# Performance work log

Hardware: AMD Instinct MI355X
Metric: run time of the kernel (lower is better)

Reference implementation:

```python
import jax, jax.numpy as jnp
import numpy as np

N, E, C, Z = 20000, 320000, 64, 10
NLM, NB, P = 9, 8, 4          # (lmax=2 -> 9 lm comps), 8 Bessel, 4 contraction paths
RMAX, AVG = 5.0, 16.0         # radial cutoff, avg_num_neighbors
L_OF_LM = jnp.array([0, 1, 1, 1, 2, 2, 2, 2, 2])  # which l each lm component belongs to


def _sph_harm(u):
    """Component-normalized real spherical harmonics, lmax=2. u: [E,3] unit vectors."""
    x, y, z = u[:, 0], u[:, 1], u[:, 2]
    s3, s5, s15 = jnp.sqrt(3.0), jnp.sqrt(5.0), jnp.sqrt(15.0)
    return jnp.stack([
        jnp.ones_like(x),
        s3 * x, s3 * y, s3 * z,
        s15 * x * y, s15 * y * z, 0.5 * s5 * (3.0 * z * z - 1.0),
        s15 * x * z, 0.5 * s15 * (x * x - y * y),
    ], axis=-1)  # [E, 9]


def _forward(positions, atomic_indices, edge_index, W_embed, W_up,
             mlp_w1, mlp_w2, mlp_w3, mlp_w4, U3, U2, U1, Wc3, Wc2, Wc1, W_out):
    sender, receiver = edge_index[0], edge_index[1]
    # edge vectors / lengths (shifts == 0)
    vec = positions[receiver] - positions[sender]               # [E,3]
    r = jnp.sqrt(jnp.sum(vec * vec, axis=-1) + 1e-12)           # [E]
    Y = _sph_harm(vec / r[:, None])                             # [E,9]
    # Bessel radial basis * polynomial cutoff (p=6)
    n = jnp.arange(1, NB + 1, dtype=positions.dtype)
    bessel = jnp.sqrt(2.0 / RMAX) * jnp.sin(n[None, :] * jnp.pi * r[:, None] / RMAX) / r[:, None]
    u = jnp.clip(r / RMAX, 0.0, 1.0)
    p = 6.0
    fcut = 1.0 - 0.5 * (p + 1) * (p + 2) * u**6 + p * (p + 2) * u**7 - 0.5 * p * (p + 1) * u**8
    edge_feats = bessel * fcut[:, None]                         # [E,8]
    # per-edge tensor-product weights: SiLU MLP, no biases (MACE FullyConnectedNet)
    f = jax.nn.silu(edge_feats @ mlp_w1)
    f = jax.nn.silu(f @ mlp_w2)
    f = jax.nn.silu(f @ mlp_w3)
    tpw = (f @ mlp_w4).reshape(-1, 3, C)                        # [E, n_l=3, C]
    # node embedding (one-hot linear) + linear_up, e3nn 1/sqrt(fan_in) norm
    h = W_embed[atomic_indices] / jnp.sqrt(jnp.asarray(Z, positions.dtype))  # [N,C]
    h = (h @ W_up) / jnp.sqrt(jnp.asarray(C, positions.dtype))               # [N,C]
    # channelwise tensor product 64x0e (x) (0e+1o+2e): gather-TP
    w_lm = tpw[:, L_OF_LM, :]                                   # [E,9,C]
    mji = h[sender][:, :, None] * jnp.swapaxes(w_lm, 1, 2) * Y[:, None, :]  # [E,C,9]
    # scatter-sum messages to receivers
    message = jax.ops.segment_sum(mji, receiver, num_segments=N) / AVG       # [N,C,9]
    x = message  # reshape() output: [N, C, lm]
    # symmetric product contraction (correlation=3), element-dependent weights
    W3n, W2n, W1n = Wc3[atomic_indices], Wc2[atomic_indices], Wc1[atomic_indices]  # [N,P,C]
    out = jnp.einsum('ijkp,npc,nci->ncjk', U3, W3n, x)          # [N,C,9,9]
    c2 = jnp.einsum('jkp,npc->ncjk', U2, W2n) + out
    out = jnp.einsum('ncjk,nck->ncj', c2, x)                    # [N,C,9]
    c1 = jnp.einsum('jp,npc->ncj', U1, W1n) + out
    out = jnp.einsum('ncj,ncj->nc', c1, x)                      # [N,C] invariant output
    return (out @ W_out) / jnp.sqrt(jnp.asarray(C, positions.dtype))


def setup_inputs() -> dict:
    key = jax.random.key(0)
    ks = jax.random.split(key, 16)
    return {
        'positions': jax.random.normal(ks[0], (N, 3), jnp.float32),
        'atomic_indices': jax.random.randint(ks[1], (N,), 0, Z),
        'edge_index': jax.random.randint(ks[2], (2, E), 0, N),
        'W_embed': jax.random.normal(ks[3], (Z, C), jnp.float32),
        'W_up': jax.random.normal(ks[4], (C, C), jnp.float32),
        'mlp_w1': jax.random.normal(ks[5], (NB, 64), jnp.float32) / np.sqrt(NB),
        'mlp_w2': jax.random.normal(ks[6], (64, 64), jnp.float32) / 8.0,
        'mlp_w3': jax.random.normal(ks[7], (64, 64), jnp.float32) / 8.0,
        'mlp_w4': jax.random.normal(ks[8], (64, 3 * C), jnp.float32) / 8.0,
        'U3': jax.random.normal(ks[9], (NLM, NLM, NLM, P), jnp.float32) * 0.1,
        'U2': jax.random.normal(ks[10], (NLM, NLM, P), jnp.float32) * 0.1,
        'U1': jax.random.normal(ks[11], (NLM, P), jnp.float32) * 0.1,
        'Wc3': jax.random.normal(ks[12], (Z, P, C), jnp.float32) * 0.1,
        'Wc2': jax.random.normal(ks[13], (Z, P, C), jnp.float32) * 0.1,
        'Wc1': jax.random.normal(ks[14], (Z, P, C), jnp.float32) * 0.1,
        'W_out': jax.random.normal(ks[15], (C, C), jnp.float32),
    }


def reference(positions, atomic_indices, edge_index, W_embed, W_up,
              mlp_w1, mlp_w2, mlp_w3, mlp_w4, U3, U2, U1, Wc3, Wc2, Wc1, W_out):
    return _forward(positions, atomic_indices, edge_index, W_embed, W_up,
                    mlp_w1, mlp_w2, mlp_w3, mlp_w4, U3, U2, U1, Wc3, Wc2, Wc1, W_out)
```

## Files before the change

### kernel.cpp

```cpp
#include <hip/hip_runtime.h>
#include <hip/hip_bf16.h>

typedef unsigned short u16;
typedef unsigned int u32;
typedef __attribute__((ext_vector_type(8))) short bf16x8;
typedef __attribute__((ext_vector_type(4))) float f32x4;

#define NN 20000
#define NE 320000

#define WP_H     256
#define WP_U1    3072
#define WP_U2    3328
#define WP_U3    4096
#define WP_CUR   7168
#define WP_POSF  87168
#define WP_WB    407168
#define WP_EL16  452224

__device__ __forceinline__ float bf2f(u16 u){ return __uint_as_float(((u32)u) << 16); }
__device__ __forceinline__ u16 f2bf(float f){
  u32 u = __float_as_uint(f);
  u32 r = (u + 0x7fffu + ((u >> 16) & 1u)) >> 16;
  return (u16)r;
}
__device__ __forceinline__ u16 f2bfa(float f){
  return (u16)((__float_as_uint(f) + 0x8000u) >> 16);
}
__device__ __forceinline__ u32 pk2bf(float a, float b){
  __hip_bfloat162 h = __float22bfloat162_rn(make_float2(a, b));
  return *(u32*)&h;
}
__device__ __forceinline__ float silu_f(float v){
  return v * __builtin_amdgcn_rcpf(1.0f + __expf(-v));
}
__device__ __forceinline__ float ldf(const void* p, int i, int bf){
  return bf ? bf2f(((const u16*)p)[i]) : ((const float*)p)[i];
}
__device__ __forceinline__ f32x4 mfma16(bf16x8 a, bf16x8 b, f32x4 c){
  return __builtin_amdgcn_mfma_f32_16x16x32_bf16(a, b, c, 0, 0, 0);
}

#define WAVE_SYNC() do { \
  __builtin_amdgcn_wave_barrier(); \
  asm volatile("s_waitcnt lgkmcnt(0)" ::: "memory"); \
  __builtin_amdgcn_wave_barrier(); \
} while (0)

#define SOFT_FENCE() do { \
  __builtin_amdgcn_wave_barrier(); \
  asm volatile("" ::: "memory"); \
  __builtin_amdgcn_wave_barrier(); \
} while (0)

__device__ __forceinline__ int sniff_wave(const u32* wu, int lane){
  u32 w = wu[lane];
  u32 e = (w >> 7) & 0xFFu;
  unsigned long long m = __ballot(e >= 0x60u && e <= 0x86u);
  return (__popcll(m) > 37) ? 1 : 0;
}

extern "C" __global__ __launch_bounds__(256)
void k_prep_pad(const void* __restrict__ We, const void* __restrict__ Wu,
                const void* __restrict__ U3, const void* __restrict__ U2, const void* __restrict__ U1,
                const void* __restrict__ w1, const void* __restrict__ w2,
                const void* __restrict__ w3, const void* __restrict__ w4,
                const void* __restrict__ pos, const int* __restrict__ eidx,
                float* __restrict__ Hws, float* __restrict__ U3ws,
                float* __restrict__ U2ws, float* __restrict__ U1ws,
                u16* __restrict__ wbws, float4* __restrict__ posf,
                int* __restrict__ cur, u16* __restrict__ el16)
{
  int tid = threadIdx.x;
  int b = blockIdx.x;
  int bf = sniff_wave((const u32*)Wu, tid & 63);

  {
    int e = b*256 + tid;
    int r = eidx[NE + e];
    int s = eidx[e];
    int slot = atomicAdd(&cur[r], 1);
    if (slot < 64) el16[(r << 6) + slot] = (u16)s;
  }

  if (b == 0){
    for (int t = tid; t < 36; t += 256) U1ws[t] = ldf(U1, t, bf);
    for (int t = tid; t < 45; t += 256){
      int j = 0, rem = t;
      for (;;){ int cnt = 9 - j; if (rem < cnt) break; rem -= cnt; ++j; }
      int k = j + rem;
      for (int p = 0; p < 4; ++p){
        float v = ldf(U2, (j*9 + k)*4 + p, bf);
        if (k > j) v += ldf(U2, (k*9 + j)*4 + p, bf);
        U2ws[t*4 + p] = v;
      }
    }
    for (int t = tid; t < 165; t += 256){
      int i = 0, rem = t;
      for (;;){ int m = 9 - i; int cnt = m*(m+1)/2; if (rem < cnt) break; rem -= cnt; ++i; }
      int j = i;
      for (;;){ int cnt = 9 - j; if (rem < cnt) break; rem -= cnt; ++j; }
      int k = j + rem;
      int pm[6][3] = {{i,j,k},{i,k,j},{j,i,k},{j,k,i},{k,i,j},{k,j,i}};
      float acc[4] = {0,0,0,0};
      for (int m = 0; m < 6; ++m){
        bool dup = false;
        for (int mm = 0; mm < m; ++mm)
          if (pm[mm][0]==pm[m][0] && pm[mm][1]==pm[m][1] && pm[mm][2]==pm[m][2]) dup = true;
        if (!dup){
          int base = ((pm[m][0]*9 + pm[m][1])*9 + pm[m][2])*4;
          for (int p = 0; p < 4; ++p) acc[p] += ldf(U3, base + p, bf);
        }
      }
      for (int p = 0; p < 4; ++p) U3ws[t*4 + p] = acc[p];
    }
  } else if (b <= 88){
    int idx = (b - 1)*256 + tid;
    int f = idx >> 9;
    int L = (idx >> 3) & 63;
    int j = idx & 7;
    int kl = ((L >> 4) << 3) + j;
    int n16 = L & 15;
    float v;
    if (f < 4){
      v = (kl < 8) ? ldf(w1, kl*64 + (f*16 + n16), bf) : 0.f;
    } else if (f < 12){
      int g = f - 4; int t = g >> 1, q = g & 1;
      v = ldf(w2, (q*32 + kl)*64 + (t*16 + n16), bf);
    } else if (f < 20){
      int g = f - 12; int t = g >> 1, q = g & 1;
      v = ldf(w3, (q*32 + kl)*64 + (t*16 + n16), bf);
    } else {
      int g = f - 20; int lt = g >> 1, q = g & 1;
      int l = lt >> 2, ct = lt & 3;
      v = ldf(w4, (q*32 + kl)*192 + (l*64 + ct*16 + n16), bf);
    }
    wbws[idx] = f2bf(v);
  } else if (b <= 167){
    int i = (b - 89)*256 + tid;
    if (i < NN){
      float4 v;
      v.x = ldf(pos, 3*i+0, bf); v.y = ldf(pos, 3*i+1, bf); v.z = ldf(pos, 3*i+2, bf); v.w = 0.f;
      posf[i] = v;
    }
  } else if (b <= 177){
    int z = b - 168;
    int c = tid;
    if (c < 64){
      float s = 0.f;
      for (int k = 0; k < 64; ++k) s += ldf(We, z*64 + k, bf) * ldf(Wu, k*64 + c, bf);
      Hws[z*64 + c] = s * 0.0395284708f;
    }
  }
}

__device__ __forceinline__ void edge_geom(float4 pr, float4 ps, float* ef, float* Y)
{
  float vx = pr.x - ps.x, vy = pr.y - ps.y, vz = pr.z - ps.z;
  float r2 = vx*vx + vy*vy + vz*vz + 1e-12f;
  float rinv = rsqrtf(r2);
  float r = r2 * rinv;
  float ux = vx*rinv, uy = vy*rinv, uz = vz*rinv;
  const float s3 = 1.7320508076f, s5 = 2.2360679775f, s15 = 3.8729833462f;
  Y[0] = 1.0f;
  Y[1] = s3*ux; Y[2] = s3*uy; Y[3] = s3*uz;
  Y[4] = s15*ux*uy; Y[5] = s15*uy*uz;
  Y[6] = 0.5f*s5*(3.0f*uz*uz - 1.0f);
  Y[7] = s15*ux*uz;
  Y[8] = 0.5f*s15*(ux*ux - uy*uy);
  float u = r * 0.2f; u = fminf(u, 1.0f);
  float u2 = u*u, u4 = u2*u2, u6 = u4*u2, u7 = u6*u, u8 = u7*u;
  float fc = 1.0f - 28.0f*u6 + 48.0f*u7 - 21.0f*u8;
  float c0 = 0.63245553203f * fc * rinv;
  float w = 0.62831853072f * r;
  #pragma unroll
  for (int k = 0; k < 8; ++k) ef[k] = c0 * __sinf(w * (float)(k + 1));
}

extern "C" __global__ __launch_bounds__(256, 3)
void k_main(const int* __restrict__ atom,
            const void* __restrict__ Wu,
            const void* __restrict__ Wc3, const void* __restrict__ Wc2, const void* __restrict__ Wc1,
            const void* __restrict__ Woutg,
            const float* __restrict__ Hws, const float* __restrict__ U3ws,
            const float* __restrict__ U2ws, const float* __restrict__ U1ws,
            const float4* __restrict__ posf,
            const int* __restrict__ deg, const u16* __restrict__ el16,
            const u16* __restrict__ wbws, void* __restrict__ outp)
{
  __shared__ __align__(16) u16   wb[12288];
  __shared__ __align__(16) float Hs[10][64];
  __shared__ __align__(16) u16   efb[4][64][8];
  __shared__ __align__(16) u16   zb64[4][64];
  __shared__ __align__(16) u16   act[4][16][64];
  __shared__ __align__(16) u16   Yc[4][64][9];
  __shared__ __align__(16) u16   pfrag[4][4][32][8];

  int tid = threadIdx.x;
  int wv = tid >> 6;
  int lane = tid & 63;
  int bf = sniff_wave((const u32*)Wu, lane);

  for (int t = tid; t < 6144; t += 256) ((u32*)wb)[t] = ((const u32*)wbws)[5120 + t];
  for (int t = tid; t < 640; t += 256) ((float*)Hs)[t] = Hws[t];
  __syncthreads();

  int c0 = lane & 15;
  int qd = lane >> 4;
  int n = blockIdx.x * 4 + wv;
  int cnt = min(deg[n], 64);
  float4 pr = posf[n];

  bf16x8 w1p[4], w2p[8], w3p[8];
  #pragma unroll
  for (int t = 0; t < 4; ++t) w1p[t] = *(const bf16x8*)&wbws[t*512 + lane*8];
  #pragma unroll
  for (int g = 0; g < 8; ++g) w2p[g] = *(const bf16x8*)&wbws[(4+g)*512 + lane*8];
  #pragma unroll
  for (int g = 0; g < 8; ++g) w3p[g] = *(const bf16x8*)&wbws[(12+g)*512 + lane*8];

  int lmap = (c0 == 0) ? 0 : (c0 < 4) ? 1 : 2;
  u32 msk0 = (lmap == 0) ? 0xFFFFFFFFu : 0u;
  u32 msk1 = (lmap == 1) ? 0xFFFFFFFFu : 0u;
  u32 msk2 = (lmap == 2) ? 0xFFFFFFFFu : 0u;

  const f32x4 zero4 = {0.f, 0.f, 0.f, 0.f};
  f32x4 XD[4];
  #pragma unroll
  for (int t = 0; t < 4; ++t) XD[t] = zero4;

  int prow = ((qd >> 1) << 4) + c0;
  int pcol = (qd & 1) << 2;
  int ntile = (cnt + 15) >> 4;

  {
    bool valid = lane < cnt;
    int sid = valid ? (int)el16[(n << 6) + lane] : n;
    float4 ps = posf[sid];
    int z = valid ? atom[sid] : 0;
    float ef[8], Y[9];
    edge_geom(pr, ps, ef, Y);
    if (!valid){
      #pragma unroll
      for (int k = 0; k < 8; ++k) ef[k] = 0.f;
      #pragma unroll
      for (int m = 0; m < 9; ++m) Y[m] = 0.f;
    }
    uint4 pk;
    pk.x = pk2bf(ef[0], ef[1]);
    pk.y = pk2bf(ef[2], ef[3]);
    pk.z = pk2bf(ef[4], ef[5]);
    pk.w = pk2bf(ef[6], ef[7]);
    *(uint4*)&efb[wv][lane][0] = pk;
    #pragma unroll
    for (int m = 0; m < 9; ++m) Yc[wv][lane][m] = f2bf(Y[m]);
    zb64[wv][lane] = (u16)z;
  }
  SOFT_FENCE();

  #pragma unroll 1
  for (int t = 0; t < ntile; ++t){
    f32x4 dd[4];

    bf16x8 aF = {0,0,0,0,0,0,0,0};
    if (lane < 16) aF = *(const bf16x8*)&efb[wv][t*16 + lane][0];
    #pragma unroll
    for (int t2 = 0; t2 < 4; ++t2) dd[t2] = mfma16(aF, w1p[t2], zero4);
    #pragma unroll
    for (int t2 = 0; t2 < 4; ++t2)
      #pragma unroll
      for (int r = 0; r < 4; ++r)
        act[wv][qd*4 + r][c0 + 16*t2] = f2bfa(silu_f(dd[t2][r]));
    SOFT_FENCE();

    bf16x8 a0 = *(const bf16x8*)&act[wv][c0][qd*8];
    bf16x8 a1 = *(const bf16x8*)&act[wv][c0][32 + qd*8];
    #pragma unroll
    for (int t2 = 0; t2 < 4; ++t2)
      dd[t2] = mfma16(a1, w2p[t2*2+1], mfma16(a0, w2p[t2*2+0], zero4));
    #pragma unroll
    for (int t2 = 0; t2 < 4; ++t2)
      #pragma unroll
      for (int r = 0; r < 4; ++r)
        act[wv][qd*4 + r][c0 + 16*t2] = f2bfa(silu_f(dd[t2][r]));
    SOFT_FENCE();

    a0 = *(const bf16x8*)&act[wv][c0][qd*8];
    a1 = *(const bf16x8*)&act[wv][c0][32 + qd*8];
    #pragma unroll
    for (int t2 = 0; t2 < 4; ++t2)
      dd[t2] = mfma16(a1, w3p[t2*2+1], mfma16(a0, w3p[t2*2+0], zero4));
    #pragma unroll
    for (int t2 = 0; t2 < 4; ++t2)
      #pragma unroll
      for (int r = 0; r < 4; ++r)
        act[wv][qd*4 + r][c0 + 16*t2] = f2bfa(silu_f(dd[t2][r]));
    SOFT_FENCE();

    a0 = *(const bf16x8*)&act[wv][c0][qd*8];
    a1 = *(const bf16x8*)&act[wv][c0][32 + qd*8];

    u32 yd0 = 0, yd1 = 0, yd2 = 0, yd3 = 0;
    if (lane < 32 && c0 < 9){
      const u16* yr = &Yc[wv][t*16 + ((lane >> 4) << 3)][0];
      yd0 = (u32)yr[0*9 + c0] | ((u32)yr[1*9 + c0] << 16);
      yd1 = (u32)yr[2*9 + c0] | ((u32)yr[3*9 + c0] << 16);
      yd2 = (u32)yr[4*9 + c0] | ((u32)yr[5*9 + c0] << 16);
      yd3 = (u32)yr[6*9 + c0] | ((u32)yr[7*9 + c0] << 16);
    }
    bf16x8 B0, B1, B2;
    { uint4 t0 = {yd0 & msk0, yd1 & msk0, yd2 & msk0, yd3 & msk0};
      uint4 t1 = {yd0 & msk1, yd1 & msk1, yd2 & msk1, yd3 & msk1};
      uint4 t2 = {yd0 & msk2, yd1 & msk2, yd2 & msk2, yd3 & msk2};
      B0 = *(bf16x8*)&t0; B1 = *(bf16x8*)&t1; B2 = *(bf16x8*)&t2; }

    float hv[4][4];
    #pragma unroll
    for (int r = 0; r < 4; ++r){
      int z_e = (int)zb64[wv][t*16 + qd*4 + r];
      #pragma unroll
      for (int ct = 0; ct < 4; ++ct) hv[r][ct] = Hs[z_e][ct*16 + c0];
    }
    #pragma unroll
    for (int l = 0; l < 3; ++l){
      #pragma unroll
      for (int ct = 0; ct < 4; ++ct){
        int f = (l*4 + ct)*2;
        bf16x8 b0 = *(const bf16x8*)&wb[f*512 + lane*8];
        bf16x8 b1 = *(const bf16x8*)&wb[(f+1)*512 + lane*8];
        dd[ct] = mfma16(a1, b1, mfma16(a0, b0, zero4));
      }
      #pragma unroll
      for (int ct = 0; ct < 4; ++ct){
        uint2 pk2;
        pk2.x = pk2bf(hv[0][ct] * dd[ct][0], hv[1][ct] * dd[ct][1]);
        pk2.y = pk2bf(hv[2][ct] * dd[ct][2], hv[3][ct] * dd[ct][3]);
        *(uint2*)&pfrag[wv][ct][prow][pcol] = pk2;
      }
      SOFT_FENCE();
      bf16x8 Bl = (l == 0) ? B0 : (l == 1) ? B1 : B2;
      #pragma unroll
      for (int ct = 0; ct < 4; ++ct){
        bf16x8 aP = {0,0,0,0,0,0,0,0};
        if (lane < 32) aP = *(const bf16x8*)&pfrag[wv][ct][lane][0];
        XD[ct] = mfma16(aP, Bl, XD[ct]);
      }
      SOFT_FENCE();
    }
  }

  float* Xf8 = (float*)&act[wv][0][0];
  float* X8f = (float*)&efb[wv][0][0];
  SOFT_FENCE();
  #pragma unroll
  for (int ct = 0; ct < 4; ++ct)
    #pragma unroll
    for (int r = 0; r < 4; ++r){
      int c = ct*16 + qd*4 + r;
      if (c0 < 8)       Xf8[c*8 + c0] = XD[ct][r];
      else if (c0 == 8) X8f[c]        = XD[ct][r];
    }
  SOFT_FENCE();
  float X[9];
  {
    const float4* xr = (const float4*)&Xf8[lane*8];
    float4 xa = xr[0], xb = xr[1];
    X[0]=xa.x; X[1]=xa.y; X[2]=xa.z; X[3]=xa.w;
    X[4]=xb.x; X[5]=xb.y; X[6]=xb.z; X[7]=xb.w;
    X[8]=X8f[lane];
  }
  #pragma unroll
  for (int m = 0; m < 9; ++m) X[m] *= 0.0625f;

  const float4* U1g = (const float4*)U1ws;
  const float4* U2g = (const float4*)U2ws;
  const float4* U3g = (const float4*)U3ws;
  float s1a[4] = {0,0,0,0}, s2a[4] = {0,0,0,0}, s3a[4] = {0,0,0,0};
  #pragma unroll
  for (int j = 0; j < 9; ++j){
    float4 u = U1g[j];
    s1a[0] += u.x*X[j]; s1a[1] += u.y*X[j]; s1a[2] += u.z*X[j]; s1a[3] += u.w*X[j];
  }
  {
    int t2i = 0;
    #pragma unroll
    for (int j = 0; j < 9; ++j)
      #pragma unroll
      for (int k = j; k < 9; ++k){
        float m = X[j]*X[k];
        float4 u = U2g[t2i]; ++t2i;
        s2a[0] += u.x*m; s2a[1] += u.y*m; s2a[2] += u.z*m; s2a[3] += u.w*m;
      }
  }
  {
    int t3i = 0;
    #pragma unroll
    for (int i = 0; i < 9; ++i)
      #pragma unroll
      for (int j = i; j < 9; ++j){
        float mij = X[i]*X[j];
        #pragma unroll
        for (int k = j; k < 9; ++k){
          float m = mij*X[k];
          float4 u = U3g[t3i]; ++t3i;
          s3a[0] += u.x*m; s3a[1] += u.y*m; s3a[2] += u.z*m; s3a[3] += u.w*m;
        }
      }
  }

  int zn = atom[n];
  float outval = 0.f;
  #pragma unroll
  for (int p = 0; p < 4; ++p){
    int b = (zn*4 + p)*64 + lane;
    outval += ldf(Wc1, b, bf)*s1a[p] + ldf(Wc2, b, bf)*s2a[p] + ldf(Wc3, b, bf)*s3a[p];
  }

  float* xchg = (float*)&act[wv][0][0];
  SOFT_FENCE();
  xchg[lane] = outval;
  SOFT_FENCE();
  float acc = 0.f;
  const float4* pb = (const float4*)xchg;
  if (bf){
    const u16* wg = (const u16*)Woutg;
    #pragma unroll
    for (int cb = 0; cb < 16; ++cb){
      float4 p = pb[cb];
      acc += p.x*bf2f(wg[(4*cb+0)*64 + lane]) + p.y*bf2f(wg[(4*cb+1)*64 + lane])
           + p.z*bf2f(wg[(4*cb+2)*64 + lane]) + p.w*bf2f(wg[(4*cb+3)*64 + lane]);
    }
  } else {
    const float* wg = (const float*)Woutg;
    #pragma unroll
    for (int cb = 0; cb < 16; ++cb){
      float4 p = pb[cb];
      acc += p.x*wg[(4*cb+0)*64 + lane] + p.y*wg[(4*cb+1)*64 + lane]
           + p.z*wg[(4*cb+2)*64 + lane] + p.w*wg[(4*cb+3)*64 + lane];
    }
  }
  acc *= 0.125f;
  if (bf) ((u16*)outp)[n*64 + lane] = f2bf(acc);
  else    ((float*)outp)[n*64 + lane] = acc;
}

extern "C" void kernel_launch(void* const* d_in, const int* in_sizes, int n_in,
                              void* d_out, int out_size, void* d_ws, size_t ws_size,
                              hipStream_t stream)
{
  const void* pos  = d_in[0];
  const int* atom  = (const int*)d_in[1];
  const int* eidx  = (const int*)d_in[2];
  const void* We   = d_in[3];
  const void* Wu   = d_in[4];
  const void* w1g  = d_in[5];
  const void* w2g  = d_in[6];
  const void* w3g  = d_in[7];
  const void* w4g  = d_in[8];
  const void* U3   = d_in[9];
  const void* U2   = d_in[10];
  const void* U1   = d_in[11];
  const void* Wc3  = d_in[12];
  const void* Wc2  = d_in[13];
  const void* Wc1  = d_in[14];
  const void* Wout = d_in[15];

  char* ws = (char*)d_ws;
  float*  Hws   = (float*)(ws + WP_H);
  float*  U1ws  = (float*)(ws + WP_U1);
  float*  U2ws  = (float*)(ws + WP_U2);
  float*  U3ws  = (float*)(ws + WP_U3);
  int*    cur   = (int*)(ws + WP_CUR);
  float4* posf  = (float4*)(ws + WP_POSF);
  u16*    wbws  = (u16*)(ws + WP_WB);
  u16*    el16  = (u16*)(ws + WP_EL16);

  (void)hipMemsetAsync(ws + WP_CUR, 0, 80000, stream);
  k_prep_pad<<<1250, 256, 0, stream>>>(We, Wu, U3, U2, U1, w1g, w2g, w3g, w4g, pos, eidx,
                                       Hws, U3ws, U2ws, U1ws, wbws, posf, cur, el16);
  k_main<<<5000, 256, 0, stream>>>(atom, Wu, Wc3, Wc2, Wc1, Wout,
                                   Hws, U3ws, U2ws, U1ws, posf,
                                   cur, el16, wbws, d_out);
}
```

Baseline: 289.2 us.

## Drop LDS weight staging, read W4 and H from global, swizzle act buffer

Removes the 24KB shared-memory copy of the fourth MLP weight matrix and the H table. Those values are now read directly from global memory, through the cache, inside the tile loop, and the block-wide syncthreads is dropped. The act scratch buffer gets an XOR swizzle to cut LDS bank conflicts, and launch bounds rise to 5 blocks per CU to raise occupancy. The trade-off is more global/L1 traffic per tile and tighter register limits, which could cause spills.

```diff
diff --git a/kernel.cpp b/kernel.cpp
--- a/kernel.cpp
+++ b/kernel.cpp
@@ -40,12 +40,6 @@
 __device__ __forceinline__ f32x4 mfma16(bf16x8 a, bf16x8 b, f32x4 c){
   return __builtin_amdgcn_mfma_f32_16x16x32_bf16(a, b, c, 0, 0, 0);
 }
-
-#define WAVE_SYNC() do { \
-  __builtin_amdgcn_wave_barrier(); \
-  asm volatile("s_waitcnt lgkmcnt(0)" ::: "memory"); \
-  __builtin_amdgcn_wave_barrier(); \
-} while (0)
 
 #define SOFT_FENCE() do { \
   __builtin_amdgcn_wave_barrier(); \
@@ -177,7 +171,7 @@
   for (int k = 0; k < 8; ++k) ef[k] = c0 * __sinf(w * (float)(k + 1));
 }
 
-extern "C" __global__ __launch_bounds__(256, 3)
+extern "C" __global__ __launch_bounds__(256, 5)
 void k_main(const int* __restrict__ atom,
             const void* __restrict__ Wu,
             const void* __restrict__ Wc3, const void* __restrict__ Wc2, const void* __restrict__ Wc1,
@@ -188,11 +182,9 @@
             const int* __restrict__ deg, const u16* __restrict__ el16,
             const u16* __restrict__ wbws, void* __restrict__ outp)
 {
-  __shared__ __align__(16) u16   wb[12288];
-  __shared__ __align__(16) float Hs[10][64];
+  __shared__ __align__(16) u16   act[4][1024];
   __shared__ __align__(16) u16   efb[4][64][8];
   __shared__ __align__(16) u16   zb64[4][64];
-  __shared__ __align__(16) u16   act[4][16][64];
   __shared__ __align__(16) u16   Yc[4][64][9];
   __shared__ __align__(16) u16   pfrag[4][4][32][8];
 
@@ -200,10 +192,6 @@
   int wv = tid >> 6;
   int lane = tid & 63;
   int bf = sniff_wave((const u32*)Wu, lane);
-
-  for (int t = tid; t < 6144; t += 256) ((u32*)wb)[t] = ((const u32*)wbws)[5120 + t];
-  for (int t = tid; t < 640; t += 256) ((float*)Hs)[t] = Hws[t];
-  __syncthreads();
 
   int c0 = lane & 15;
   int qd = lane >> 4;
@@ -211,6 +199,10 @@
   int cnt = min(deg[n], 64);
   float4 pr = posf[n];
 
+  u16* A = &act[wv][0];
+  int swr = qd << 4;
+  int srd = (c0 >> 2) << 4;
+
   bf16x8 w1p[4], w2p[8], w3p[8];
   #pragma unroll
   for (int t = 0; t < 4; ++t) w1p[t] = *(const bf16x8*)&wbws[t*512 + lane*8];
@@ -218,6 +210,8 @@
   for (int g = 0; g < 8; ++g) w2p[g] = *(const bf16x8*)&wbws[(4+g)*512 + lane*8];
   #pragma unroll
   for (int g = 0; g < 8; ++g) w3p[g] = *(const bf16x8*)&wbws[(12+g)*512 + lane*8];
+
+  const u16* w4b = wbws + 20*512 + lane*8;
 
   int lmap = (c0 == 0) ? 0 : (c0 < 4) ? 1 : 2;
   u32 msk0 = (lmap == 0) ? 0xFFFFFFFFu : 0u;
@@ -270,11 +264,11 @@
     for (int t2 = 0; t2 < 4; ++t2)
       #pragma unroll
       for (int r = 0; r < 4; ++r)
-        act[wv][qd*4 + r][c0 + 16*t2] = f2bfa(silu_f(dd[t2][r]));
+        A[(((qd*4 + r) << 6) + c0 + (t2 << 4)) ^ swr] = f2bfa(silu_f(dd[t2][r]));
     SOFT_FENCE();
 
-    bf16x8 a0 = *(const bf16x8*)&act[wv][c0][qd*8];
-    bf16x8 a1 = *(const bf16x8*)&act[wv][c0][32 + qd*8];
+    bf16x8 a0 = *(const bf16x8*)&A[((c0 << 6) + (qd << 3)) ^ srd];
+    bf16x8 a1 = *(const bf16x8*)&A[((c0 << 6) + 32 + (qd << 3)) ^ srd];
     #pragma unroll
     for (int t2 = 0; t2 < 4; ++t2)
       dd[t2] = mfma16(a1, w2p[t2*2+1], mfma16(a0, w2p[t2*2+0], zero4));
@@ -282,11 +276,11 @@
     for (int t2 = 0; t2 < 4; ++t2)
       #pragma unroll
       for (int r = 0; r < 4; ++r)
-        act[wv][qd*4 + r][c0 + 16*t2] = f2bfa(silu_f(dd[t2][r]));
+        A[(((qd*4 + r) << 6) + c0 + (t2 << 4)) ^ swr] = f2bfa(silu_f(dd[t2][r]));
     SOFT_FENCE();
 
-    a0 = *(const bf16x8*)&act[wv][c0][qd*8];
-    a1 = *(const bf16x8*)&act[wv][c0][32 + qd*8];
+    a0 = *(const bf16x8*)&A[((c0 << 6) + (qd << 3)) ^ srd];
+    a1 = *(const bf16x8*)&A[((c0 << 6) + 32 + (qd << 3)) ^ srd];
     #pragma unroll
     for (int t2 = 0; t2 < 4; ++t2)
       dd[t2] = mfma16(a1, w3p[t2*2+1], mfma16(a0, w3p[t2*2+0], zero4));
@@ -294,11 +288,11 @@
     for (int t2 = 0; t2 < 4; ++t2)
       #pragma unroll
       for (int r = 0; r < 4; ++r)
-        act[wv][qd*4 + r][c0 + 16*t2] = f2bfa(silu_f(dd[t2][r]));
+        A[(((qd*4 + r) << 6) + c0 + (t2 << 4)) ^ swr] = f2bfa(silu_f(dd[t2][r]));
     SOFT_FENCE();
 
-    a0 = *(const bf16x8*)&act[wv][c0][qd*8];
-    a1 = *(const bf16x8*)&act[wv][c0][32 + qd*8];
+    a0 = *(const bf16x8*)&A[((c0 << 6) + (qd << 3)) ^ srd];
+    a1 = *(const bf16x8*)&A[((c0 << 6) + 32 + (qd << 3)) ^ srd];
 
     u32 yd0 = 0, yd1 = 0, yd2 = 0, yd3 = 0;
     if (lane < 32 && c0 < 9){
@@ -319,15 +313,15 @@
     for (int r = 0; r < 4; ++r){
       int z_e = (int)zb64[wv][t*16 + qd*4 + r];
       #pragma unroll
-      for (int ct = 0; ct < 4; ++ct) hv[r][ct] = Hs[z_e][ct*16 + c0];
+      for (int ct = 0; ct < 4; ++ct) hv[r][ct] = Hws[z_e*64 + ct*16 + c0];
     }
     #pragma unroll
     for (int l = 0; l < 3; ++l){
       #pragma unroll
       for (int ct = 0; ct < 4; ++ct){
         int f = (l*4 + ct)*2;
-        bf16x8 b0 = *(const bf16x8*)&wb[f*512 + lane*8];
-        bf16x8 b1 = *(const bf16x8*)&wb[(f+1)*512 + lane*8];
+        bf16x8 b0 = *(const bf16x8*)&w4b[f*512];
+        bf16x8 b1 = *(const bf16x8*)&w4b[(f+1)*512];
         dd[ct] = mfma16(a1, b1, mfma16(a0, b0, zero4));
       }
       #pragma unroll
@@ -349,7 +343,7 @@
     }
   }
 
-  float* Xf8 = (float*)&act[wv][0][0];
+  float* Xf8 = (float*)A;
   float* X8f = (float*)&efb[wv][0][0];
   SOFT_FENCE();
   #pragma unroll
@@ -416,7 +410,7 @@
     outval += ldf(Wc1, b, bf)*s1a[p] + ldf(Wc2, b, bf)*s2a[p] + ldf(Wc3, b, bf)*s3a[p];
   }
 
-  float* xchg = (float*)&act[wv][0][0];
+  float* xchg = (float*)A;
   SOFT_FENCE();
   xchg[lane] = outval;
   SOFT_FENCE();
```

Measured after the change: 440.2 us. 1.52x slower.
